# Optimization experiments

Hardware: AMD Instinct MI355X
Metric: run time of the kernel (lower is better)

The kernel has to match this reference:

```python
import jax, jax.numpy as jnp
import numpy as np

N_NODES = 100000
N_EDGES = 1600000
IN_CH, HID, EMB = 128, 64, 32


def _glorot(key, shape):
    lim = np.sqrt(6.0 / (shape[0] + shape[1])).astype(np.float32)
    return jax.random.uniform(key, shape, jnp.float32, -lim, lim)


def setup_inputs() -> dict:
    key = jax.random.key(0)
    ks = jax.random.split(key, 5)
    x = jax.random.normal(ks[0], (N_NODES, IN_CH), dtype=jnp.float32)
    edges = jax.random.randint(ks[1], (2, N_EDGES), 0, N_NODES)
    W1 = _glorot(ks[2], (IN_CH, HID)); b1 = jnp.zeros((HID,), jnp.float32)
    W2 = _glorot(ks[3], (HID, EMB)); b2 = jnp.zeros((EMB,), jnp.float32)
    W3 = _glorot(ks[4], (HID, EMB)); b3 = jnp.zeros((EMB,), jnp.float32)
    return {"x": x, "edges": edges, "W1": W1, "b1": b1,
            "W2": W2, "b2": b2, "W3": W3, "b3": b3}


def reference(x, edges, W1, b1, W2, b2, W3, b3):
    N = x.shape[0]
    # GCNConv default: add self-loops, symmetric D^-1/2 A D^-1/2 normalization
    loop = jnp.arange(N, dtype=edges.dtype)
    src = jnp.concatenate([edges[0], loop])  # [E+N] message sources
    dst = jnp.concatenate([edges[1], loop])  # [E+N] message targets
    deg = jax.ops.segment_sum(jnp.ones_like(dst, dtype=x.dtype), dst, num_segments=N)
    dinv = jnp.where(deg > 0, jax.lax.rsqrt(deg), 0.0)
    norm = dinv[src] * dinv[dst]  # [E+N], cached across the three convs (cached=True)

    def gcn(h, W, b):
        h = h @ W                                  # [N, out]
        msg = h[src] * norm[:, None]               # gather + edge scale
        return jax.ops.segment_sum(msg, dst, num_segments=N) + b  # scatter-add

    h = jax.nn.relu(gcn(x, W1, b1))
    return gcn(h, W2, b2), gcn(h, W3, b3)
```

## Files before the change

kernel.cpp:

```cpp
#include <hip/hip_runtime.h>

#define NN 100000
#define NE 1600000
#define NB 391
#define CHUNK 4096
#define NCHUNK 391

typedef __attribute__((ext_vector_type(8))) short short8_t;
typedef __attribute__((ext_vector_type(4))) float float4_t;

__device__ inline unsigned short f2bf(float f) {
    unsigned int u = __float_as_uint(f);
    unsigned int r = u + 0x7fffu + ((u >> 16) & 1u);
    return (unsigned short)(r >> 16);
}
__device__ inline float bf_lo(unsigned int u) { return __uint_as_float(u << 16); }
__device__ inline float bf_hi(unsigned int u) { return __uint_as_float(u & 0xffff0000u); }

__global__ __launch_bounds__(256) void k_pre(const float* __restrict__ W1,
                                             const float* __restrict__ W2,
                                             const float* __restrict__ W3,
                                             unsigned short* __restrict__ wtb,
                                             unsigned short* __restrict__ wt2,
                                             int* __restrict__ bhist) {
    int f = blockIdx.x * 256 + threadIdx.x;
    int c = f >> 7, k = f & 127;
    wtb[f] = f2bf(W1[k * 64 + c]);
    if (f < 4096) {
        int c2 = f >> 6, k2 = f & 63;
        float v = (c2 < 32) ? W2[k2 * 32 + c2] : W3[k2 * 32 + (c2 - 32)];
        wt2[f] = f2bf(v);
    }
    if (f < NB) bhist[f] = 0;
}

__global__ __launch_bounds__(256) void k_hist(const int* __restrict__ dst,
                                              int* __restrict__ bhist) {
    __shared__ int lh[NB];
    int t = threadIdx.x;
    for (int i = t; i < NB; i += 256) lh[i] = 0;
    __syncthreads();
    for (int e = blockIdx.x * 256 + t; e < NE; e += 256 * 256)
        atomicAdd(&lh[dst[e] >> 8], 1);
    __syncthreads();
    for (int i = t; i < NB; i += 256)
        if (lh[i]) atomicAdd(&bhist[i], lh[i]);
}

__global__ __launch_bounds__(256) void k_scanb(const int* __restrict__ bhist,
                                               int* __restrict__ boff,
                                               int* __restrict__ bcur) {
    __shared__ int sh[256];
    int t = threadIdx.x;
    int base = t * 2;
    int v0 = (base + 0 < NB) ? bhist[base + 0] : 0;
    int v1 = (base + 1 < NB) ? bhist[base + 1] : 0;
    int tsum = v0 + v1;
    sh[t] = tsum;
    __syncthreads();
    for (int d = 1; d < 256; d <<= 1) {
        int x = (t >= d) ? sh[t - d] : 0;
        __syncthreads();
        sh[t] += x;
        __syncthreads();
    }
    int excl = sh[t] - tsum;
    if (base + 0 < NB) { boff[base + 0] = excl;      bcur[base + 0] = excl; }
    if (base + 1 < NB) { boff[base + 1] = excl + v0; bcur[base + 1] = excl + v0; }
    if (t == 255) boff[NB] = sh[255];
}

__global__ __launch_bounds__(512) void k_fuse(const float* __restrict__ x,
                                              const unsigned short* __restrict__ wtb,
                                              unsigned short* __restrict__ t1b,
                                              const int* __restrict__ src,
                                              const int* __restrict__ dst,
                                              int* __restrict__ bcur,
                                              unsigned int* __restrict__ pairs) {
    __shared__ int sbuf[2 * NB];
    const int b = blockIdx.x;
    const int t = threadIdx.x;

    if ((b % 3) == 2) {
        int* lh    = sbuf;
        int* lbase = sbuf + NB;
        int e0 = (b / 3) * CHUNK;
        int e1 = min(e0 + CHUNK, NE);
        for (int i = t; i < NB; i += 512) lh[i] = 0;
        __syncthreads();
        for (int e = e0 + t; e < e1; e += 512)
            atomicAdd(&lh[dst[e] >> 8], 1);
        __syncthreads();
        int rot = (int)(((unsigned)(b / 3) * 97u) % NB);
        for (int i = t; i < NB; i += 512) {
            int ii = i + rot; if (ii >= NB) ii -= NB;
            int h = lh[ii];
            lbase[ii] = h ? atomicAdd(&bcur[ii], h) : 0;
        }
        __syncthreads();
        for (int i = t; i < NB; i += 512) lh[i] = 0;
        __syncthreads();
        for (int e = e0 + t; e < e1; e += 512) {
            int d = dst[e];
            int bk = d >> 8;
            int r = atomicAdd(&lh[bk], 1);
            pairs[lbase[bk] + r] = (unsigned int)src[e] | ((unsigned int)(d & 255) << 17);
        }
    } else {
        const int tile = 2 * (b / 3) + (b % 3);
        const int row0 = tile * 128;
        const int nrows = min(128, NN - row0);
        const int w = t >> 6, l = t & 63;
        const int m15 = l & 15, kg = l >> 4;

        int ra = min(row0 + w * 16 + m15, NN - 1);
        const float* xa = x + (size_t)ra * 128 + kg * 8;

        float4_t acc[4];
        #pragma unroll
        for (int cb = 0; cb < 4; ++cb) acc[cb] = (float4_t){0.f, 0.f, 0.f, 0.f};

        #pragma unroll
        for (int ks = 0; ks < 4; ++ks) {
            float4 f0 = *(const float4*)(xa + ks * 32);
            float4 f1 = *(const float4*)(xa + ks * 32 + 4);
            short8_t a;
            a[0] = (short)f2bf(f0.x); a[1] = (short)f2bf(f0.y);
            a[2] = (short)f2bf(f0.z); a[3] = (short)f2bf(f0.w);
            a[4] = (short)f2bf(f1.x); a[5] = (short)f2bf(f1.y);
            a[6] = (short)f2bf(f1.z); a[7] = (short)f2bf(f1.w);
            #pragma unroll
            for (int cb = 0; cb < 4; ++cb) {
                short8_t bb = *(const short8_t*)(wtb + (cb * 16 + m15) * 128 + ks * 32 + kg * 8);
                acc[cb] = __builtin_amdgcn_mfma_f32_16x16x32_bf16(a, bb, acc[cb], 0, 0, 0);
            }
        }

        #pragma unroll
        for (int r = 0; r < 4; ++r) {
            int lrow = w * 16 + kg * 4 + r;
            if (lrow < nrows) {
                size_t grow = (size_t)(row0 + lrow);
                #pragma unroll
                for (int cb = 0; cb < 4; ++cb)
                    t1b[grow * 64 + cb * 16 + m15] = f2bf(acc[cb][r]);
            }
        }
    }
}

__global__ __launch_bounds__(256) void k_fine(const unsigned int* __restrict__ pairs,
                                              const int* __restrict__ boff,
                                              int* __restrict__ csr_off,
                                              int* __restrict__ csr_src,
                                              float* __restrict__ dinv) {
    __shared__ int lcnt[256];
    __shared__ int sc[256];
    __shared__ int lofs[256];
    int t = threadIdx.x;
    int b = blockIdx.x;
    int n0 = b << 8;
    int nnode = min(256, NN - n0);
    int bO = boff[b], bE = boff[b + 1];

    lcnt[t] = 0;
    __syncthreads();
    for (int e = bO + t; e < bE; e += 256)
        atomicAdd(&lcnt[pairs[e] >> 17], 1);
    __syncthreads();
    sc[t] = lcnt[t];
    __syncthreads();
    for (int d = 1; d < 256; d <<= 1) {
        int x = (t >= d) ? sc[t - d] : 0;
        __syncthreads();
        sc[t] += x;
        __syncthreads();
    }
    {
        int excl = sc[t] - lcnt[t];
        lofs[t] = excl;
        if (t < nnode) {
            int n = n0 + t;
            csr_off[n] = bO + excl;
            dinv[n] = rsqrtf(1.0f + (float)lcnt[t]);
        }
        lcnt[t] = 0;
    }
    if (b == NB - 1 && t == 0) csr_off[NN] = NE;
    __syncthreads();
    for (int e = bO + t; e < bE; e += 256) {
        unsigned int w = pairs[e];
        int li = (int)(w >> 17);
        int r = atomicAdd(&lcnt[li], 1);
        csr_src[bO + lofs[li] + r] = (int)(w & 0x1FFFFu);
    }
}

__global__ __launch_bounds__(256) void k_gather8(const int* __restrict__ off,
                                                 const int* __restrict__ csr,
                                                 const float* __restrict__ dinv,
                                                 const unsigned short* __restrict__ hb,
                                                 const float* __restrict__ bias,
                                                 unsigned int* __restrict__ outp) {
    int idx = blockIdx.x * 256 + threadIdx.x;
    int n = idx >> 3;
    if (n >= NN) return;
    int c8 = idx & 7;
    const uint4* h4 = (const uint4*)hb;
    float dn = dinv[n];
    float a0[8], a1[8];
    {
        uint4 v = h4[(size_t)n * 8 + c8];
        a0[0] = dn * bf_lo(v.x); a0[1] = dn * bf_hi(v.x);
        a0[2] = dn * bf_lo(v.y); a0[3] = dn * bf_hi(v.y);
        a0[4] = dn * bf_lo(v.z); a0[5] = dn * bf_hi(v.z);
        a0[6] = dn * bf_lo(v.w); a0[7] = dn * bf_hi(v.w);
        #pragma unroll
        for (int j = 0; j < 8; ++j) a1[j] = 0.f;
    }
    int b = off[n], e = off[n + 1];
    int i = b;
    for (; i + 1 < e; i += 2) {
        int s0 = csr[i], s1 = csr[i + 1];
        float w0 = dinv[s0], w1 = dinv[s1];
        uint4 v0 = h4[(size_t)s0 * 8 + c8];
        uint4 v1 = h4[(size_t)s1 * 8 + c8];
        a0[0] += w0 * bf_lo(v0.x); a0[1] += w0 * bf_hi(v0.x);
        a0[2] += w0 * bf_lo(v0.y); a0[3] += w0 * bf_hi(v0.y);
        a0[4] += w0 * bf_lo(v0.z); a0[5] += w0 * bf_hi(v0.z);
        a0[6] += w0 * bf_lo(v0.w); a0[7] += w0 * bf_hi(v0.w);
        a1[0] += w1 * bf_lo(v1.x); a1[1] += w1 * bf_hi(v1.x);
        a1[2] += w1 * bf_lo(v1.y); a1[3] += w1 * bf_hi(v1.y);
        a1[4] += w1 * bf_lo(v1.z); a1[5] += w1 * bf_hi(v1.z);
        a1[6] += w1 * bf_lo(v1.w); a1[7] += w1 * bf_hi(v1.w);
    }
    if (i < e) {
        int s = csr[i];
        float w = dinv[s];
        uint4 v = h4[(size_t)s * 8 + c8];
        a0[0] += w * bf_lo(v.x); a0[1] += w * bf_hi(v.x);
        a0[2] += w * bf_lo(v.y); a0[3] += w * bf_hi(v.y);
        a0[4] += w * bf_lo(v.z); a0[5] += w * bf_hi(v.z);
        a0[6] += w * bf_lo(v.w); a0[7] += w * bf_hi(v.w);
    }
    float4 b0 = ((const float4*)bias)[c8 * 2];
    float4 b1v = ((const float4*)bias)[c8 * 2 + 1];
    float o[8];
    o[0] = dn * fmaxf(dn * (a0[0] + a1[0]) + b0.x, 0.f);
    o[1] = dn * fmaxf(dn * (a0[1] + a1[1]) + b0.y, 0.f);
    o[2] = dn * fmaxf(dn * (a0[2] + a1[2]) + b0.z, 0.f);
    o[3] = dn * fmaxf(dn * (a0[3] + a1[3]) + b0.w, 0.f);
    o[4] = dn * fmaxf(dn * (a0[4] + a1[4]) + b1v.x, 0.f);
    o[5] = dn * fmaxf(dn * (a0[5] + a1[5]) + b1v.y, 0.f);
    o[6] = dn * fmaxf(dn * (a0[6] + a1[6]) + b1v.z, 0.f);
    o[7] = dn * fmaxf(dn * (a0[7] + a1[7]) + b1v.w, 0.f);
    uint4 p;
    p.x = (unsigned int)f2bf(o[0]) | ((unsigned int)f2bf(o[1]) << 16);
    p.y = (unsigned int)f2bf(o[2]) | ((unsigned int)f2bf(o[3]) << 16);
    p.z = (unsigned int)f2bf(o[4]) | ((unsigned int)f2bf(o[5]) << 16);
    p.w = (unsigned int)f2bf(o[6]) | ((unsigned int)f2bf(o[7]) << 16);
    ((uint4*)outp)[(size_t)n * 8 + c8] = p;
}

__global__ __launch_bounds__(512) void k_gemm23(const unsigned short* __restrict__ h1b,
                                                const unsigned short* __restrict__ wt2,
                                                unsigned short* __restrict__ y) {
    __shared__ __align__(16) unsigned short lx[128 * 72];
    __shared__ __align__(16) unsigned short lw[64 * 72];
    const int t = threadIdx.x;
    const int row0 = blockIdx.x * 128;
    const int nrows = min(128, NN - row0);

    #pragma unroll
    for (int i = 0; i < 2; ++i) {
        int f = t + i * 512;
        int r = f >> 3, c8 = f & 7;
        uint4 v = make_uint4(0u, 0u, 0u, 0u);
        if (r < nrows) v = ((const uint4*)h1b)[(size_t)(row0 + r) * 8 + c8];
        *(uint4*)&lx[r * 72 + c8 * 8] = v;
    }
    if (t < 512) {
        int c = t >> 3, c8 = t & 7;
        uint4 v = ((const uint4*)wt2)[t];
        *(uint4*)&lw[c * 72 + c8 * 8] = v;
    }
    __syncthreads();

    const int w = t >> 6, l = t & 63;
    const int m15 = l & 15, kg = l >> 4;
    const unsigned short* pa = &lx[(w * 16 + m15) * 72 + kg * 8];
    const unsigned short* pb = &lw[m15 * 72 + kg * 8];

    float4_t acc[4];
    #pragma unroll
    for (int cb = 0; cb < 4; ++cb) acc[cb] = (float4_t){0.f, 0.f, 0.f, 0.f};

    #pragma unroll
    for (int ks = 0; ks < 2; ++ks) {
        short8_t a = *(const short8_t*)(pa + ks * 32);
        #pragma unroll
        for (int cb = 0; cb < 4; ++cb) {
            short8_t bb = *(const short8_t*)(pb + cb * (16 * 72) + ks * 32);
            acc[cb] = __builtin_amdgcn_mfma_f32_16x16x32_bf16(a, bb, acc[cb], 0, 0, 0);
        }
    }

    #pragma unroll
    for (int r = 0; r < 4; ++r) {
        int lrow = w * 16 + kg * 4 + r;
        if (lrow < nrows) {
            size_t grow = (size_t)(row0 + lrow);
            #pragma unroll
            for (int cb = 0; cb < 4; ++cb)
                y[grow * 64 + cb * 16 + m15] = f2bf(acc[cb][r]);
        }
    }
}

__global__ __launch_bounds__(256) void k_gatherO(const int* __restrict__ off,
                                                 const int* __restrict__ csr,
                                                 const float* __restrict__ dinv,
                                                 const unsigned short* __restrict__ yb,
                                                 const float* __restrict__ b2,
                                                 const float* __restrict__ b3,
                                                 float* __restrict__ out) {
    int idx = blockIdx.x * 256 + threadIdx.x;
    int n = idx >> 3;
    int c8 = idx & 7;
    const uint4* h4 = (const uint4*)yb;
    float a0[8], a1[8];
    {
        uint4 v = h4[(size_t)n * 8 + c8];
        a0[0] = bf_lo(v.x); a0[1] = bf_hi(v.x);
        a0[2] = bf_lo(v.y); a0[3] = bf_hi(v.y);
        a0[4] = bf_lo(v.z); a0[5] = bf_hi(v.z);
        a0[6] = bf_lo(v.w); a0[7] = bf_hi(v.w);
        #pragma unroll
        for (int j = 0; j < 8; ++j) a1[j] = 0.f;
    }
    int b = off[n], e = off[n + 1];
    int i = b;
    for (; i + 1 < e; i += 2) {
        int s0 = csr[i], s1 = csr[i + 1];
        uint4 v0 = h4[(size_t)s0 * 8 + c8];
        uint4 v1 = h4[(size_t)s1 * 8 + c8];
        a0[0] += bf_lo(v0.x); a0[1] += bf_hi(v0.x);
        a0[2] += bf_lo(v0.y); a0[3] += bf_hi(v0.y);
        a0[4] += bf_lo(v0.z); a0[5] += bf_hi(v0.z);
        a0[6] += bf_lo(v0.w); a0[7] += bf_hi(v0.w);
        a1[0] += bf_lo(v1.x); a1[1] += bf_hi(v1.x);
        a1[2] += bf_lo(v1.y); a1[3] += bf_hi(v1.y);
        a1[4] += bf_lo(v1.z); a1[5] += bf_hi(v1.z);
        a1[6] += bf_lo(v1.w); a1[7] += bf_hi(v1.w);
    }
    if (i < e) {
        uint4 v = h4[(size_t)csr[i] * 8 + c8];
        a0[0] += bf_lo(v.x); a0[1] += bf_hi(v.x);
        a0[2] += bf_lo(v.y); a0[3] += bf_hi(v.y);
        a0[4] += bf_lo(v.z); a0[5] += bf_hi(v.z);
        a0[6] += bf_lo(v.w); a0[7] += bf_hi(v.w);
    }
    float dn = dinv[n];
    const float* bp = (c8 < 4) ? (b2 + c8 * 8) : (b3 + (c8 - 4) * 8);
    float4 q0 = *(const float4*)bp;
    float4 q1 = *(const float4*)(bp + 4);
    float4 o0, o1;
    o0.x = dn * (a0[0] + a1[0]) + q0.x;
    o0.y = dn * (a0[1] + a1[1]) + q0.y;
    o0.z = dn * (a0[2] + a1[2]) + q0.z;
    o0.w = dn * (a0[3] + a1[3]) + q0.w;
    o1.x = dn * (a0[4] + a1[4]) + q1.x;
    o1.y = dn * (a0[5] + a1[5]) + q1.y;
    o1.z = dn * (a0[6] + a1[6]) + q1.z;
    o1.w = dn * (a0[7] + a1[7]) + q1.w;
    float* op = (c8 < 4) ? (out + (size_t)n * 32 + c8 * 8)
                         : (out + (size_t)NN * 32 + (size_t)n * 32 + (c8 - 4) * 8);
    *(float4*)op = o0;
    *(float4*)(op + 4) = o1;
}

extern "C" void kernel_launch(void* const* d_in, const int* in_sizes, int n_in,
                              void* d_out, int out_size, void* d_ws, size_t ws_size,
                              hipStream_t stream) {
    const float* x  = (const float*)d_in[0];
    const int* edges = (const int*)d_in[1];
    const float* W1 = (const float*)d_in[2];
    const float* b1 = (const float*)d_in[3];
    const float* W2 = (const float*)d_in[4];
    const float* b2 = (const float*)d_in[5];
    const float* W3 = (const float*)d_in[6];
    const float* b3 = (const float*)d_in[7];
    float* out = (float*)d_out;

    const int* srcs = edges;
    const int* dsts = edges + NE;

    int*   csr_off = (int*)d_ws;
    float* dinv    = (float*)((int*)d_ws + 100004);
    int*   csr_src = (int*)d_ws + 200004;
    int*   bhist   = (int*)d_ws + 1800004;
    int*   boff    = (int*)d_ws + 1800396;
    int*   bcur    = (int*)d_ws + 1800788;
    unsigned short* wtb = (unsigned short*)((int*)d_ws + 1801184);
    unsigned short* t1b = (unsigned short*)((int*)d_ws + 1805280);
    unsigned short* y   = t1b;
    unsigned int*   pairs = (unsigned int*)((int*)d_ws + 5005280);
    unsigned short* h1b   = (unsigned short*)pairs;
    unsigned short* wt2 = (unsigned short*)(out + 6400000 - 2048);

    dim3 blk(256);
    const int gN8 = (NN * 8 + 255) / 256;
    const int gT23 = (NN + 127) / 128;

    k_pre<<<32, blk, 0, stream>>>(W1, W2, W3, wtb, wt2, bhist);
    k_hist<<<256, blk, 0, stream>>>(dsts, bhist);
    k_scanb<<<1, blk, 0, stream>>>(bhist, boff, bcur);

    k_fuse<<<3 * NCHUNK, dim3(512), 0, stream>>>(x, wtb, t1b, srcs, dsts, bcur, pairs);

    k_fine<<<NB, blk, 0, stream>>>(pairs, boff, csr_off, csr_src, dinv);

    k_gather8<<<gN8, blk, 0, stream>>>(csr_off, csr_src, dinv, t1b, b1,
                                       (unsigned int*)h1b);
    k_gemm23<<<gT23, dim3(512), 0, stream>>>(h1b, wt2, y);
    k_gatherO<<<gN8, blk, 0, stream>>>(csr_off, csr_src, dinv, y, b2, b3, out);
}
```

Baseline: 151.8 us.

## Replace global atomic bucket cursors with per-chunk histogram and column scan

New measurement: 189.1 us. 24.5% more time.

```diff
diff --git a/kernel.cpp b/kernel.cpp
--- a/kernel.cpp
+++ b/kernel.cpp
@@ -21,8 +21,7 @@
                                              const float* __restrict__ W2,
                                              const float* __restrict__ W3,
                                              unsigned short* __restrict__ wtb,
-                                             unsigned short* __restrict__ wt2,
-                                             int* __restrict__ bhist) {
+                                             unsigned short* __restrict__ wt2) {
     int f = blockIdx.x * 256 + threadIdx.x;
     int c = f >> 7, k = f & 127;
     wtb[f] = f2bf(W1[k * 64 + c]);
@@ -31,30 +30,51 @@
         float v = (c2 < 32) ? W2[k2 * 32 + c2] : W3[k2 * 32 + (c2 - 32)];
         wt2[f] = f2bf(v);
     }
-    if (f < NB) bhist[f] = 0;
-}
-
-__global__ __launch_bounds__(256) void k_hist(const int* __restrict__ dst,
-                                              int* __restrict__ bhist) {
+}
+
+__global__ __launch_bounds__(256) void k_chist(const int* __restrict__ dst,
+                                               int* __restrict__ hist2d) {
     __shared__ int lh[NB];
-    int t = threadIdx.x;
+    int c = blockIdx.x, t = threadIdx.x;
     for (int i = t; i < NB; i += 256) lh[i] = 0;
     __syncthreads();
-    for (int e = blockIdx.x * 256 + t; e < NE; e += 256 * 256)
+    int e0 = c * CHUNK, e1 = min(e0 + CHUNK, NE);
+    for (int e = e0 + t; e < e1; e += 256)
         atomicAdd(&lh[dst[e] >> 8], 1);
     __syncthreads();
-    for (int i = t; i < NB; i += 256)
-        if (lh[i]) atomicAdd(&bhist[i], lh[i]);
-}
-
-__global__ __launch_bounds__(256) void k_scanb(const int* __restrict__ bhist,
-                                               int* __restrict__ boff,
-                                               int* __restrict__ bcur) {
+    for (int i = t; i < NB; i += 256) hist2d[c * NB + i] = lh[i];
+}
+
+__global__ __launch_bounds__(256) void k_scancol(const int* __restrict__ hist2d,
+                                                 int* __restrict__ base2d,
+                                                 int* __restrict__ colsum) {
+    __shared__ int sh[256];
+    int b = blockIdx.x, t = threadIdx.x;
+    int base = t * 2;
+    int v0 = (base + 0 < NCHUNK) ? hist2d[(base + 0) * NB + b] : 0;
+    int v1 = (base + 1 < NCHUNK) ? hist2d[(base + 1) * NB + b] : 0;
+    int tsum = v0 + v1;
+    sh[t] = tsum;
+    __syncthreads();
+    for (int d = 1; d < 256; d <<= 1) {
+        int x = (t >= d) ? sh[t - d] : 0;
+        __syncthreads();
+        sh[t] += x;
+        __syncthreads();
+    }
+    int excl = sh[t] - tsum;
+    if (base + 0 < NCHUNK) base2d[(base + 0) * NB + b] = excl;
+    if (base + 1 < NCHUNK) base2d[(base + 1) * NB + b] = excl + v0;
+    if (t == 255) colsum[b] = sh[255];
+}
+
+__global__ __launch_bounds__(256) void k_scanb(const int* __restrict__ colsum,
+                                               int* __restrict__ boff) {
     __shared__ int sh[256];
     int t = threadIdx.x;
     int base = t * 2;
-    int v0 = (base + 0 < NB) ? bhist[base + 0] : 0;
-    int v1 = (base + 1 < NB) ? bhist[base + 1] : 0;
+    int v0 = (base + 0 < NB) ? colsum[base + 0] : 0;
+    int v1 = (base + 1 < NB) ? colsum[base + 1] : 0;
     int tsum = v0 + v1;
     sh[t] = tsum;
     __syncthreads();
@@ -65,8 +85,8 @@
         __syncthreads();
     }
     int excl = sh[t] - tsum;
-    if (base + 0 < NB) { boff[base + 0] = excl;      bcur[base + 0] = excl; }
-    if (base + 1 < NB) { boff[base + 1] = excl + v0; bcur[base + 1] = excl + v0; }
+    if (base + 0 < NB) boff[base + 0] = excl;
+    if (base + 1 < NB) boff[base + 1] = excl + v0;
     if (t == 255) boff[NB] = sh[255];
 }
 
@@ -75,30 +95,23 @@
                                               unsigned short* __restrict__ t1b,
                                               const int* __restrict__ src,
                                               const int* __restrict__ dst,
-                                              int* __restrict__ bcur,
+                                              const int* __restrict__ base2d,
+                                              const int* __restrict__ boff,
                                               unsigned int* __restrict__ pairs) {
     __shared__ int sbuf[2 * NB];
     const int b = blockIdx.x;
     const int t = threadIdx.x;
 
     if ((b % 3) == 2) {
-        int* lh    = sbuf;
-        int* lbase = sbuf + NB;
-        int e0 = (b / 3) * CHUNK;
+        int* lbase = sbuf;
+        int* lh    = sbuf + NB;
+        const int c = b / 3;
+        int e0 = c * CHUNK;
         int e1 = min(e0 + CHUNK, NE);
-        for (int i = t; i < NB; i += 512) lh[i] = 0;
-        __syncthreads();
-        for (int e = e0 + t; e < e1; e += 512)
-            atomicAdd(&lh[dst[e] >> 8], 1);
-        __syncthreads();
-        int rot = (int)(((unsigned)(b / 3) * 97u) % NB);
         for (int i = t; i < NB; i += 512) {
-            int ii = i + rot; if (ii >= NB) ii -= NB;
-            int h = lh[ii];
-            lbase[ii] = h ? atomicAdd(&bcur[ii], h) : 0;
-        }
-        __syncthreads();
-        for (int i = t; i < NB; i += 512) lh[i] = 0;
+            lbase[i] = base2d[c * NB + i] + boff[i];
+            lh[i] = 0;
+        }
         __syncthreads();
         for (int e = e0 + t; e < e1; e += 512) {
             int d = dst[e];
@@ -398,25 +411,28 @@
     int*   csr_off = (int*)d_ws;
     float* dinv    = (float*)((int*)d_ws + 100004);
     int*   csr_src = (int*)d_ws + 200004;
-    int*   bhist   = (int*)d_ws + 1800004;
+    int*   colsum  = (int*)d_ws + 1800004;
     int*   boff    = (int*)d_ws + 1800396;
-    int*   bcur    = (int*)d_ws + 1800788;
-    unsigned short* wtb = (unsigned short*)((int*)d_ws + 1801184);
-    unsigned short* t1b = (unsigned short*)((int*)d_ws + 1805280);
+    unsigned short* wtb = (unsigned short*)((int*)d_ws + 1800788);
+    unsigned short* t1b = (unsigned short*)((int*)d_ws + 1804884);
     unsigned short* y   = t1b;
-    unsigned int*   pairs = (unsigned int*)((int*)d_ws + 5005280);
-    unsigned short* h1b   = (unsigned short*)pairs;
+    unsigned int*   pairs  = (unsigned int*)((int*)d_ws + 5004884);
+    int*            hist2d = (int*)d_ws + 5004884 + 1600000;
+    int*            base2d = (int*)d_ws + 5004884 + 1752881;
+    unsigned short* h1b    = (unsigned short*)pairs;
     unsigned short* wt2 = (unsigned short*)(out + 6400000 - 2048);
 
     dim3 blk(256);
     const int gN8 = (NN * 8 + 255) / 256;
     const int gT23 = (NN + 127) / 128;
 
-    k_pre<<<32, blk, 0, stream>>>(W1, W2, W3, wtb, wt2, bhist);
-    k_hist<<<256, blk, 0, stream>>>(dsts, bhist);
-    k_scanb<<<1, blk, 0, stream>>>(bhist, boff, bcur);
-
-    k_fuse<<<3 * NCHUNK, dim3(512), 0, stream>>>(x, wtb, t1b, srcs, dsts, bcur, pairs);
+    k_pre<<<32, blk, 0, stream>>>(W1, W2, W3, wtb, wt2);
+    k_chist<<<NCHUNK, blk, 0, stream>>>(dsts, hist2d);
+    k_scancol<<<NB, blk, 0, stream>>>(hist2d, base2d, colsum);
+    k_scanb<<<1, blk, 0, stream>>>(colsum, boff);
+
+    k_fuse<<<3 * NCHUNK, dim3(512), 0, stream>>>(x, wtb, t1b, srcs, dsts,
+                                                 base2d, boff, pairs);
 
     k_fine<<<NB, blk, 0, stream>>>(pairs, boff, csr_off, csr_src, dinv);
 
```
